# Optimization experiments

Measured on AMD Instinct MI355X. Metric: run time of the kernel, lower is better.

The kernel has to match this reference:

```python
import jax, jax.numpy as jnp
import numpy as np

N_USERS = 50000
N_ITEMS = 50000
N_NODES = N_USERS + N_ITEMS
EMBED_DIM = 64
N_INTER = 2_000_000
SSL_RATIO = 0.5
SSL_TEMP = 0.5
SSL_REG = 0.5
BATCH = 2048


def _make_subgraph(tu, ti, seed):
    """Edge-dropout (aug_type=1) + symmetric normalization, as COO arrays."""
    rng = np.random.default_rng(seed)
    keep = rng.choice(N_INTER, int(N_INTER * (1.0 - SSL_RATIO)), replace=False)
    u = tu[keep]
    i = ti[keep] + N_USERS
    rows = np.concatenate([u, i])          # symmetrize: A + A^T
    cols = np.concatenate([i, u])
    deg = np.bincount(rows, minlength=N_NODES).astype(np.float32)
    dinv = np.where(deg > 0, 1.0 / np.sqrt(deg), 0.0).astype(np.float32)
    vals = dinv[rows] * dinv[cols]         # D^-1/2 A D^-1/2
    return (jnp.asarray(rows, jnp.int32), jnp.asarray(cols, jnp.int32),
            jnp.asarray(vals, jnp.float32))


def setup_inputs() -> dict:
    key = jax.random.key(0)
    k1, k2, k3, k4 = jax.random.split(key, 4)
    rng = np.random.default_rng(0)
    tu = rng.integers(0, N_USERS, N_INTER)
    ti = rng.integers(0, N_ITEMS, N_INTER)
    rows1, cols1, vals1 = _make_subgraph(tu, ti, 1)
    rows2, cols2, vals2 = _make_subgraph(tu, ti, 2)
    return {
        "user_emb": jax.random.normal(k1, (N_USERS, EMBED_DIM), jnp.float32) * 0.1,
        "item_emb": jax.random.normal(k2, (N_ITEMS, EMBED_DIM), jnp.float32) * 0.1,
        "rows1": rows1, "cols1": cols1, "vals1": vals1,
        "rows2": rows2, "cols2": cols2, "vals2": vals2,
        "nodes_u": jax.random.randint(k3, (BATCH,), 0, N_USERS, jnp.int32),
        "nodes_i": jax.random.randint(k4, (BATCH,), 0, N_ITEMS, jnp.int32),
    }


def _spmm(rows, cols, vals, x):
    # sparse (n_nodes x n_nodes) @ dense (n_nodes x d) via gather + segment_sum
    return jax.ops.segment_sum(vals[:, None] * x[cols], rows, num_segments=N_NODES)


def _l2norm(x):
    return x / jnp.maximum(jnp.linalg.norm(x, axis=1, keepdims=True), 1e-12)


def _info_nce(emb1_all, emb2_all, idx, temp):
    z1 = _l2norm(emb1_all[idx])            # [B, d]
    z2 = _l2norm(emb2_all[idx])            # [B, d]
    zall = _l2norm(emb2_all)               # [N, d]
    pos = jnp.exp(jnp.sum(z1 * z2, axis=1) / temp)           # [B]
    ttl = jnp.sum(jnp.exp(jnp.dot(z1, zall.T) / temp), axis=1)  # [B]
    return -jnp.sum(jnp.log(pos / ttl))


def reference(user_emb, item_emb, rows1, cols1, vals1, rows2, cols2, vals2,
              nodes_u, nodes_i):
    ego = jnp.concatenate([user_emb, item_emb], axis=0)   # [N_NODES, d]
    # NOTE: in the original source the propagation matmul sits *after* the
    # layer loop (indentation bug), so exactly one SpMM layer is applied and
    # the stacked mean is (ego + A @ ego) / 2. We reproduce that faithfully.
    e1 = 0.5 * (ego + _spmm(rows1, cols1, vals1, ego))
    e2 = 0.5 * (ego + _spmm(rows2, cols2, vals2, ego))
    u1, i1 = e1[:N_USERS], e1[N_USERS:]
    u2, i2 = e2[:N_USERS], e2[N_USERS:]
    ssl_loss_user = _info_nce(u1, u2, nodes_u, SSL_TEMP)
    ssl_loss_item = _info_nce(i1, i2, nodes_i, SSL_TEMP)
    return SSL_REG * (ssl_loss_user + ssl_loss_item)
```

## Files before the change

### kernel.cpp

```cpp
#include <hip/hip_runtime.h>
#include <hip/hip_bf16.h>
#include <hip/hip_fp16.h>
#include <math.h>

#define N_USERS 50000
#define N_ITEMS 50000
#define N_NODES 100000
#define DIM 64
#define BATCH 2048
#define SLOTS 4096

#define BROWS 128
#define NBUK 782
#define CAPB 4096
#define SUBCAP 1024
#define BCHUNK 8192
#define BINTHREADS 1024

#define TTL_PRESCALE 2.8853900817779268f

using frag_ab = __attribute__((ext_vector_type(8))) short;
using frag_cd = __attribute__((ext_vector_type(4))) float;
typedef unsigned long long u64;
typedef unsigned int u32;


__device__ __forceinline__ float wave_reduce_sum(float v) {
#pragma unroll
  for (int off = 32; off > 0; off >>= 1)
    v += __shfl_xor(v, off, 64);
  return v;
}

__device__ __forceinline__ const float* ego_row(const float* ue, const float* ie, int n) {
  return (n < N_USERS) ? (ue + (size_t)n * DIM) : (ie + (size_t)(n - N_USERS) * DIM);
}

__device__ __forceinline__ ushort f2bf(float x) {
  __hip_bfloat16 h = __float2bfloat16(x);
  return *(ushort*)&h;
}

__device__ __forceinline__ float bf2f(ushort u) {
  return __uint_as_float(((unsigned)u) << 16);
}

__device__ __forceinline__ float exp2_native(float x) {
  float y;
  asm volatile("v_exp_f32 %0, %1" : "=v"(y) : "v"(x));
  return y;
}


__global__ void build_map_kernel(const int* __restrict__ nu, const int* __restrict__ ni,
                                 int* __restrict__ map) {
  int s = blockIdx.x * blockDim.x + threadIdx.x;
  if (s >= SLOTS) return;
  int n = (s < BATCH) ? nu[s] : (N_USERS + ni[s - BATCH]);
  map[n] = s;
}

__global__ __launch_bounds__(BINTHREADS) void bin_kernel(
    const int* __restrict__ rows, const int* __restrict__ cols,
    int* __restrict__ bcur, u32* __restrict__ rec, int nE) {
  __shared__ int lofs[NBUK];
  int tid = threadIdx.x;
  int sub = blockIdx.x & 3;
  int e0 = blockIdx.x * BCHUNK;
  int nHere = nE - e0;
  if (nHere > BCHUNK) nHere = BCHUNK;

  for (int i = tid; i < NBUK; i += BINTHREADS) lofs[i] = 0;
  __syncthreads();

  for (int i = tid; i < nHere; i += BINTHREADS)
    atomicAdd(&lofs[rows[e0 + i] >> 7], 1);
  __syncthreads();

  for (int b = tid; b < NBUK; b += BINTHREADS) {
    int c = lofs[b];
    lofs[b] = c ? atomicAdd(&bcur[(b * 4 + sub) * 16], c) : 0;
  }
  __syncthreads();

  for (int i = tid; i < nHere; i += BINTHREADS) {
    int r = rows[e0 + i];
    int b = r >> 7;
    int p = atomicAdd(&lofs[b], 1);
    if (p < SUBCAP)
      rec[((size_t)b << 12) + sub * SUBCAP + p] =
          ((u32)(r & 127) << 17) | (u32)cols[e0 + i];
  }
}

__global__ __launch_bounds__(256) void sort_kernel(
    const int* __restrict__ bcur, const u32* __restrict__ rec,
    u32* __restrict__ rec2, int* __restrict__ base, int* __restrict__ endv) {
  __shared__ int hist[BROWS];
  __shared__ int hcur[BROWS];
  int b = blockIdx.x;
  int tid = threadIdx.x;
  int cnt[4];
#pragma unroll
  for (int j = 0; j < 4; j++) {
    int c = bcur[(b * 4 + j) * 16];
    cnt[j] = (c < SUBCAP) ? c : SUBCAP;
  }
  size_t gb = (size_t)b << 12;

  if (tid < BROWS) hist[tid] = 0;
  __syncthreads();

  u32 myrec[CAPB / 256];
#pragma unroll
  for (int i = 0; i < CAPB / 256; i++) {
    int k = tid + i * 256;
    u32 u = ((k & (SUBCAP - 1)) < cnt[i >> 2]) ? rec[gb + k] : ~0u;
    myrec[i] = u;
    if (u != ~0u) atomicAdd(&hist[(u >> 17) & 127], 1);
  }
  __syncthreads();

  int wave = tid >> 6, lane = tid & 63;
  if (wave == 0) {
    int v0 = hist[lane], v1 = hist[lane + 64];
    int s0 = v0, s1 = v1;
#pragma unroll
    for (int off = 1; off < 64; off <<= 1) {
      int t0 = __shfl_up(s0, off, 64);
      if (lane >= off) s0 += t0;
      int t1 = __shfl_up(s1, off, 64);
      if (lane >= off) s1 += t1;
    }
    int tot0 = __shfl(s0, 63, 64);
    int e0 = s0 - v0;
    int e1 = tot0 + s1 - v1;
    hcur[lane] = e0;
    hcur[lane + 64] = e1;
    int gb32 = b * CAPB;
    int n0 = b * BROWS;
    if (n0 + lane < N_NODES) {
      base[n0 + lane] = gb32 + e0;
      endv[n0 + lane] = gb32 + e0 + v0;
    }
    if (n0 + lane + 64 < N_NODES) {
      base[n0 + lane + 64] = gb32 + e1;
      endv[n0 + lane + 64] = gb32 + e1 + v1;
    }
  }
  __syncthreads();

#pragma unroll
  for (int i = 0; i < CAPB / 256; i++) {
    u32 u = myrec[i];
    if (u != ~0u) {
      int rl = (u >> 17) & 127;
      int pos = atomicAdd(&hcur[rl], 1);
      rec2[gb + pos] = u & 0x1FFFF;
    }
  }
}

__global__ void ego2bf_kernel(const float* __restrict__ ue, const float* __restrict__ ie,
                              const int* __restrict__ base, const int* __restrict__ endv,
                              ushort* __restrict__ xb, ushort* __restrict__ xbp) {
  int t = blockIdx.x * blockDim.x + threadIdx.x;
  const int TOT = N_NODES * DIM / 4;
  if (t >= TOT) return;
  const int UH = N_USERS * DIM / 4;
  float4 f = (t < UH) ? ((const float4*)ue)[t] : ((const float4*)ie)[t - UH];
  ushort4 o;
  o.x = f2bf(f.x); o.y = f2bf(f.y); o.z = f2bf(f.z); o.w = f2bf(f.w);
  ((ushort4*)xb)[t] = o;
  int node = t >> 4;
  int d = endv[node] - base[node];
  float dc = (d > 0) ? rsqrtf((float)d) : 0.f;
  ushort4 p;
  p.x = f2bf(f.x * dc); p.y = f2bf(f.y * dc); p.z = f2bf(f.z * dc); p.w = f2bf(f.w * dc);
  ((ushort4*)xbp)[t] = p;
}

__global__ __launch_bounds__(256) void spmm_csr_norm_kernel(
    const int* __restrict__ base, const int* __restrict__ endv,
    const u32* __restrict__ rec2, const ushort* __restrict__ xbp,
    const float* __restrict__ ue, const float* __restrict__ ie,
    ushort* __restrict__ zallb) {
  int n = blockIdx.x * 4 + (threadIdx.x >> 6);
  if (n >= N_NODES) return;
  int lane = threadIdx.x & 63;
  int half = lane >> 5;
  int sl = lane & 31;
  int b = base[n];
  int d = endv[n] - b;
  const u32* rp = rec2 + b;
  float a0 = 0.f, a1 = 0.f;
  int k = half;
  for (; k + 6 < d; k += 8) {
    u32 c0 = rp[k], c1 = rp[k + 2], c2 = rp[k + 4], c3 = rp[k + 6];
    u32 u0 = *(const u32*)(xbp + ((size_t)c0 << 6) + 2 * sl);
    u32 u1 = *(const u32*)(xbp + ((size_t)c1 << 6) + 2 * sl);
    u32 u2 = *(const u32*)(xbp + ((size_t)c2 << 6) + 2 * sl);
    u32 u3 = *(const u32*)(xbp + ((size_t)c3 << 6) + 2 * sl);
    a0 += (__uint_as_float(u0 << 16) + __uint_as_float(u1 << 16)) +
          (__uint_as_float(u2 << 16) + __uint_as_float(u3 << 16));
    a1 += (__uint_as_float(u0 & 0xFFFF0000u) + __uint_as_float(u1 & 0xFFFF0000u)) +
          (__uint_as_float(u2 & 0xFFFF0000u) + __uint_as_float(u3 & 0xFFFF0000u));
  }
  for (; k < d; k += 2) {
    u32 c = rp[k];
    u32 u = *(const u32*)(xbp + ((size_t)c << 6) + 2 * sl);
    a0 += __uint_as_float(u << 16);
    a1 += __uint_as_float(u & 0xFFFF0000u);
  }
  a0 += __shfl_xor(a0, 32, 64);
  a1 += __shfl_xor(a1, 32, 64);

  float dinv = (d > 0) ? rsqrtf((float)d) : 0.f;
  a0 *= dinv;
  a1 *= dinv;

  const float* eg = ego_row(ue, ie, n);
  float2 e2 = *(const float2*)(eg + 2 * sl);
  float w0 = 0.5f * (e2.x + a0);
  float w1 = 0.5f * (e2.y + a1);
  float ss = w0 * w0 + w1 * w1;
#pragma unroll
  for (int off = 16; off > 0; off >>= 1)
    ss += __shfl_xor(ss, off, 64);
  float inv = 1.f / fmaxf(sqrtf(ss), 1e-12f);
  if (half == 0) {
    ushort2 oz;
    oz.x = f2bf(w0 * inv);
    oz.y = f2bf(w1 * inv);
    *(ushort2*)(zallb + (size_t)n * DIM + 2 * sl) = oz;
  }
}

__global__ __launch_bounds__(256) void graph1_fused_kernel(
    const int* __restrict__ rows, const int* __restrict__ cols,
    const float* __restrict__ vals, const int* __restrict__ map,
    const ushort* __restrict__ xb, float* __restrict__ z1acc, int nE) {
  __shared__ int lcount;
  __shared__ int hcol[256];
  __shared__ float hval[256];
  __shared__ int hslot[256];
  int tid = threadIdx.x;
  if (tid == 0) lcount = 0;
  __syncthreads();
  int e = blockIdx.x * 256 + tid;
  if (e < nE) {
    int r = rows[e];
    int s = map[r];
    if (s >= 0) {
      int pos = atomicAdd(&lcount, 1);
      hcol[pos] = cols[e];
      hval[pos] = vals[e];
      hslot[pos] = s;
    }
  }
  __syncthreads();
  int n = lcount;
  int wave = tid >> 6, lane = tid & 63;
  for (int k = wave; k < n; k += 4) {
    int c = hcol[k];
    float v = hval[k];
    int s = hslot[k];
    float x = bf2f(xb[(size_t)c * DIM + lane]);
    unsafeAtomicAdd(&z1acc[(size_t)s * DIM + lane], v * x);
  }
}

__global__ void gather1_kernel(const float* __restrict__ ue, const float* __restrict__ ie,
                               const int* __restrict__ nu, const int* __restrict__ ni,
                               const int* __restrict__ map, const float* __restrict__ z1acc,
                               const ushort* __restrict__ zallb, ushort* __restrict__ z1b,
                               float* __restrict__ posdot) {
  int s = blockIdx.x * 4 + (threadIdx.x >> 6);
  if (s >= SLOTS) return;
  int lane = threadIdx.x & 63;
  int n = (s < BATCH) ? nu[s] : (N_USERS + ni[s - BATCH]);
  int fs = map[n];
  const float* e = ego_row(ue, ie, n);
  float v = 0.5f * (e[lane] + z1acc[(size_t)fs * DIM + lane]);
  float ss = wave_reduce_sum(v * v);
  float z = v / fmaxf(sqrtf(ss), 1e-12f);
  z1b[(size_t)s * DIM + lane] = f2bf(z * TTL_PRESCALE);
  float dp = wave_reduce_sum(z * bf2f(zallb[(size_t)n * DIM + lane]));
  if (lane == 0) posdot[s] = dp;
}

#define TTL_STRIPS 125
#define TTL_CHUNKS 25
#define TTL_RB 16
__global__ __launch_bounds__(512) void ttl_mfma_kernel(const ushort* __restrict__ z1b,
                                                       const ushort* __restrict__ zallb,
                                                       float* __restrict__ partial) {
  __shared__ int4 sB[TTL_CHUNKS * 128];
  int bid = blockIdx.x;
  int strip = (bid & 7) + 8 * (bid >> 7);
  int rb = (bid >> 3) & 15;
  if (strip >= TTL_STRIPS) return;
  int tid = threadIdx.x;
  int wave = tid >> 6, lane = tid & 63;
  int r0 = rb * 256 + wave * 32;
  int side = (rb * 256) >> 11;
  const ushort* zs = zallb + (size_t)side * N_USERS * DIM;

  int m = lane & 15, q = lane >> 4;
  const ushort* ar0 = z1b + (size_t)(r0 + m) * DIM + q * 8;
  frag_ab a00 = *(const frag_ab*)ar0;
  frag_ab a01 = *(const frag_ab*)(ar0 + 32);
  const ushort* ar1 = ar0 + 16 * DIM;
  frag_ab a10 = *(const frag_ab*)ar1;
  frag_ab a11 = *(const frag_ab*)(ar1 + 32);

  int j0 = strip * (TTL_CHUNKS * 16);
  const char* bbase = (const char*)(zs + (size_t)j0 * DIM);

  for (int i = tid; i < TTL_CHUNKS * 128; i += 512) {
    int off = i * 16;
    int swz = off ^ (((off >> 7) & 7) << 4);
    *(int4*)((char*)sB + swz) = *(const int4*)(bbase + off);
  }
  __syncthreads();

  int swl = (m & 7) << 4;
  int o0 = (m * 128 + q * 16) ^ swl;
  int o1 = (m * 128 + 64 + q * 16) ^ swl;

  float racc[8] = {0.f, 0.f, 0.f, 0.f, 0.f, 0.f, 0.f, 0.f};

  for (int c = 0; c < TTL_CHUNKS; c++) {
    const char* sb = (const char*)sB + c * 2048;
    frag_ab b0 = *(const frag_ab*)(sb + o0);
    frag_ab b1 = *(const frag_ab*)(sb + o1);
    frag_cd acc0 = {}, acc1 = {};
    acc0 = __builtin_amdgcn_mfma_f32_16x16x32_bf16(a00, b0, acc0, 0, 0, 0);
    acc0 = __builtin_amdgcn_mfma_f32_16x16x32_bf16(a01, b1, acc0, 0, 0, 0);
    acc1 = __builtin_amdgcn_mfma_f32_16x16x32_bf16(a10, b0, acc1, 0, 0, 0);
    acc1 = __builtin_amdgcn_mfma_f32_16x16x32_bf16(a11, b1, acc1, 0, 0, 0);
#pragma unroll
    for (int r = 0; r < 4; r++) {
      racc[r] += exp2_native(acc0[r]);
      racc[4 + r] += exp2_native(acc1[r]);
    }
  }

  float* pw = partial + (size_t)strip * SLOTS;
#pragma unroll
  for (int h = 0; h < 2; h++) {
#pragma unroll
    for (int r = 0; r < 4; r++) {
      float v = racc[h * 4 + r];
      v += __shfl_xor(v, 1, 64);
      v += __shfl_xor(v, 2, 64);
      v += __shfl_xor(v, 4, 64);
      v += __shfl_xor(v, 8, 64);
      if (m == 0) pw[r0 + h * 16 + q * 4 + r] = v;
    }
  }
}

__global__ void final_kernel(const float* __restrict__ partial,
                             const float* __restrict__ posdot,
                             float* __restrict__ out) {
  int row = blockIdx.x * blockDim.x + threadIdx.x;
  float t = 0.f;
  for (int s = 0; s < TTL_STRIPS; s++)
    t += partial[(size_t)s * SLOTS + row];
  float v = 0.5f * logf(t) - posdot[row];
  v = wave_reduce_sum(v);
  if ((threadIdx.x & 63) == 0) atomicAdd(out, v);
}


extern "C" void kernel_launch(void* const* d_in, const int* in_sizes, int n_in,
                              void* d_out, int out_size, void* d_ws, size_t ws_size,
                              hipStream_t stream) {
  const float* ue = (const float*)d_in[0];
  const float* ie = (const float*)d_in[1];
  const int* rows1 = (const int*)d_in[2];
  const int* cols1 = (const int*)d_in[3];
  const float* vals1 = (const float*)d_in[4];
  const int* rows2 = (const int*)d_in[5];
  const int* cols2 = (const int*)d_in[6];
  const int* nu = (const int*)d_in[8];
  const int* ni = (const int*)d_in[9];
  int nE1 = in_sizes[2], nE2 = in_sizes[5];

  char* ws = (char*)d_ws;
  size_t o = 0;
  auto carve = [&](size_t bytes) {
    char* p = ws + o;
    o += (bytes + 255) & ~(size_t)255;
    return p;
  };
  int* map = (int*)carve(N_NODES * 4);
  float* z1acc = (float*)carve((size_t)SLOTS * DIM * 4);
  float* partial = (float*)carve((size_t)TTL_STRIPS * SLOTS * 4);
  float* posdot = (float*)carve(SLOTS * 4);
  ushort* zallb = (ushort*)carve((size_t)N_NODES * DIM * 2);
  ushort* z1b = (ushort*)carve((size_t)SLOTS * DIM * 2);
  ushort* xb = (ushort*)carve((size_t)N_NODES * DIM * 2);
  ushort* xbp = (ushort*)carve((size_t)N_NODES * DIM * 2);
  int* bcur = (int*)carve((size_t)NBUK * 4 * 16 * 4);
  int* base = (int*)carve(N_NODES * 4);
  int* endv = (int*)carve(N_NODES * 4);
  u32* rec = (u32*)carve((size_t)NBUK * CAPB * 4);
  u32* rec2 = (u32*)carve((size_t)NBUK * CAPB * 4);
  float* out = (float*)d_out;

  hipMemsetAsync(map, 0xFF, N_NODES * 4, stream);
  hipMemsetAsync(bcur, 0, (size_t)NBUK * 4 * 16 * 4, stream);
  hipMemsetAsync(z1acc, 0, (size_t)SLOTS * DIM * 4, stream);
  hipMemsetAsync(out, 0, sizeof(float), stream);

  build_map_kernel<<<16, 256, 0, stream>>>(nu, ni, map);
  bin_kernel<<<(nE2 + BCHUNK - 1) / BCHUNK, BINTHREADS, 0, stream>>>(rows2, cols2, bcur, rec, nE2);
  sort_kernel<<<NBUK, 256, 0, stream>>>(bcur, rec, rec2, base, endv);
  ego2bf_kernel<<<(N_NODES * DIM / 4 + 255) / 256, 256, 0, stream>>>(ue, ie, base, endv, xb, xbp);
  spmm_csr_norm_kernel<<<(N_NODES + 3) / 4, 256, 0, stream>>>(base, endv, rec2, xbp, ue, ie, zallb);
  graph1_fused_kernel<<<(nE1 + 255) / 256, 256, 0, stream>>>(rows1, cols1, vals1, map, xb, z1acc, nE1);
  gather1_kernel<<<SLOTS / 4, 256, 0, stream>>>(ue, ie, nu, ni, map, z1acc, zallb, z1b, posdot);
  ttl_mfma_kernel<<<2048, 512, 0, stream>>>(z1b, zallb, partial);
  final_kernel<<<SLOTS / 256, 256, 0, stream>>>(partial, posdot, out);
}
```

Measured before the change: 315.2 us.

## Merge bf16 conversion into binning, scaling into sort, and graph1 into SpMM launch

The separate ego-to-bf16 kernel is removed. The plain bf16 conversion now runs as extra blocks of the binning launch, and the degree-scaled copy is produced at the tail of the sort kernel from the per-row histogram it already holds. The graph-1 gather/atomic kernel is merged into the graph-2 CSR SpMM launch as additional blocks, so the two independent workloads can overlap. This cuts two launches and the endv/base reads in the conversion step. In exchange, xbp is now rounded to bf16 twice, and the fused launches mix block types with different shared-memory needs.

```diff
diff --git a/kernel.cpp b/kernel.cpp
--- a/kernel.cpp
+++ b/kernel.cpp
@@ -16,8 +16,11 @@
 #define SUBCAP 1024
 #define BCHUNK 8192
 #define BINTHREADS 1024
+#define XB_BLOCKS 1563
 
 #define TTL_PRESCALE 2.8853900817779268f
+
+#define SPMM_BLOCKS (N_NODES / 4)
 
 using frag_ab = __attribute__((ext_vector_type(8))) short;
 using frag_cd = __attribute__((ext_vector_type(4))) float;
@@ -60,9 +63,24 @@
   map[n] = s;
 }
 
-__global__ __launch_bounds__(BINTHREADS) void bin_kernel(
+__global__ __launch_bounds__(BINTHREADS) void bin_xb_kernel(
     const int* __restrict__ rows, const int* __restrict__ cols,
-    int* __restrict__ bcur, u32* __restrict__ rec, int nE) {
+    const float* __restrict__ ue, const float* __restrict__ ie,
+    int* __restrict__ bcur, u32* __restrict__ rec, ushort* __restrict__ xb,
+    int nE, int nBin) {
+  if ((int)blockIdx.x >= nBin) {
+    int t = (blockIdx.x - nBin) * BINTHREADS + threadIdx.x;
+    const int TOT = N_NODES * DIM / 4;
+    if (t < TOT) {
+      const int UH = N_USERS * DIM / 4;
+      float4 f = (t < UH) ? ((const float4*)ue)[t] : ((const float4*)ie)[t - UH];
+      ushort4 o;
+      o.x = f2bf(f.x); o.y = f2bf(f.y); o.z = f2bf(f.z); o.w = f2bf(f.w);
+      ((ushort4*)xb)[t] = o;
+    }
+    return;
+  }
+
   __shared__ int lofs[NBUK];
   int tid = threadIdx.x;
   int sub = blockIdx.x & 3;
@@ -95,7 +113,8 @@
 
 __global__ __launch_bounds__(256) void sort_kernel(
     const int* __restrict__ bcur, const u32* __restrict__ rec,
-    u32* __restrict__ rec2, int* __restrict__ base, int* __restrict__ endv) {
+    u32* __restrict__ rec2, int* __restrict__ base, int* __restrict__ endv,
+    const ushort* __restrict__ xb, ushort* __restrict__ xbp) {
   __shared__ int hist[BROWS];
   __shared__ int hcur[BROWS];
   int b = blockIdx.x;
@@ -159,35 +178,72 @@
       rec2[gb + pos] = u & 0x1FFFF;
     }
   }
-}
-
-__global__ void ego2bf_kernel(const float* __restrict__ ue, const float* __restrict__ ie,
-                              const int* __restrict__ base, const int* __restrict__ endv,
-                              ushort* __restrict__ xb, ushort* __restrict__ xbp) {
-  int t = blockIdx.x * blockDim.x + threadIdx.x;
-  const int TOT = N_NODES * DIM / 4;
-  if (t >= TOT) return;
-  const int UH = N_USERS * DIM / 4;
-  float4 f = (t < UH) ? ((const float4*)ue)[t] : ((const float4*)ie)[t - UH];
-  ushort4 o;
-  o.x = f2bf(f.x); o.y = f2bf(f.y); o.z = f2bf(f.z); o.w = f2bf(f.w);
-  ((ushort4*)xb)[t] = o;
-  int node = t >> 4;
-  int d = endv[node] - base[node];
-  float dc = (d > 0) ? rsqrtf((float)d) : 0.f;
-  ushort4 p;
-  p.x = f2bf(f.x * dc); p.y = f2bf(f.y * dc); p.z = f2bf(f.z * dc); p.w = f2bf(f.w * dc);
-  ((ushort4*)xbp)[t] = p;
-}
-
-__global__ __launch_bounds__(256) void spmm_csr_norm_kernel(
+
+  int r = tid >> 1;
+  int n = b * BROWS + r;
+  if (n < N_NODES) {
+    int dg = hist[r];
+    float dc = (dg > 0) ? rsqrtf((float)dg) : 0.f;
+    const ushort4* src = (const ushort4*)(xb + (size_t)n * DIM + (tid & 1) * 32);
+    ushort4* dst = (ushort4*)(xbp + (size_t)n * DIM + (tid & 1) * 32);
+#pragma unroll
+    for (int j = 0; j < 8; j++) {
+      ushort4 v = src[j];
+      ushort4 p;
+      p.x = f2bf(bf2f(v.x) * dc);
+      p.y = f2bf(bf2f(v.y) * dc);
+      p.z = f2bf(bf2f(v.z) * dc);
+      p.w = f2bf(bf2f(v.w) * dc);
+      dst[j] = p;
+    }
+  }
+}
+
+__global__ __launch_bounds__(256) void spmm_graph1_kernel(
     const int* __restrict__ base, const int* __restrict__ endv,
     const u32* __restrict__ rec2, const ushort* __restrict__ xbp,
     const float* __restrict__ ue, const float* __restrict__ ie,
-    ushort* __restrict__ zallb) {
-  int n = blockIdx.x * 4 + (threadIdx.x >> 6);
+    ushort* __restrict__ zallb,
+    const int* __restrict__ rows1, const int* __restrict__ cols1,
+    const float* __restrict__ vals1, const int* __restrict__ map,
+    const ushort* __restrict__ xb, float* __restrict__ z1acc, int nE1) {
+  __shared__ int lcount;
+  __shared__ int hcol[256];
+  __shared__ float hval[256];
+  __shared__ int hslot[256];
+  int bid = blockIdx.x;
+  int tid = threadIdx.x;
+
+  if (bid >= SPMM_BLOCKS) {
+    if (tid == 0) lcount = 0;
+    __syncthreads();
+    int e = (bid - SPMM_BLOCKS) * 256 + tid;
+    if (e < nE1) {
+      int r = rows1[e];
+      int s = map[r];
+      if (s >= 0) {
+        int pos = atomicAdd(&lcount, 1);
+        hcol[pos] = cols1[e];
+        hval[pos] = vals1[e];
+        hslot[pos] = s;
+      }
+    }
+    __syncthreads();
+    int cnt = lcount;
+    int wave = tid >> 6, lane = tid & 63;
+    for (int k = wave; k < cnt; k += 4) {
+      int c = hcol[k];
+      float v = hval[k];
+      int s = hslot[k];
+      float x = bf2f(xb[(size_t)c * DIM + lane]);
+      unsafeAtomicAdd(&z1acc[(size_t)s * DIM + lane], v * x);
+    }
+    return;
+  }
+
+  int n = bid * 4 + (tid >> 6);
   if (n >= N_NODES) return;
-  int lane = threadIdx.x & 63;
+  int lane = tid & 63;
   int half = lane >> 5;
   int sl = lane & 31;
   int b = base[n];
@@ -233,40 +289,6 @@
     oz.x = f2bf(w0 * inv);
     oz.y = f2bf(w1 * inv);
     *(ushort2*)(zallb + (size_t)n * DIM + 2 * sl) = oz;
-  }
-}
-
-__global__ __launch_bounds__(256) void graph1_fused_kernel(
-    const int* __restrict__ rows, const int* __restrict__ cols,
-    const float* __restrict__ vals, const int* __restrict__ map,
-    const ushort* __restrict__ xb, float* __restrict__ z1acc, int nE) {
-  __shared__ int lcount;
-  __shared__ int hcol[256];
-  __shared__ float hval[256];
-  __shared__ int hslot[256];
-  int tid = threadIdx.x;
-  if (tid == 0) lcount = 0;
-  __syncthreads();
-  int e = blockIdx.x * 256 + tid;
-  if (e < nE) {
-    int r = rows[e];
-    int s = map[r];
-    if (s >= 0) {
-      int pos = atomicAdd(&lcount, 1);
-      hcol[pos] = cols[e];
-      hval[pos] = vals[e];
-      hslot[pos] = s;
-    }
-  }
-  __syncthreads();
-  int n = lcount;
-  int wave = tid >> 6, lane = tid & 63;
-  for (int k = wave; k < n; k += 4) {
-    int c = hcol[k];
-    float v = hval[k];
-    int s = hslot[k];
-    float x = bf2f(xb[(size_t)c * DIM + lane]);
-    unsafeAtomicAdd(&z1acc[(size_t)s * DIM + lane], v * x);
   }
 }
 
@@ -416,11 +438,13 @@
   hipMemsetAsync(out, 0, sizeof(float), stream);
 
   build_map_kernel<<<16, 256, 0, stream>>>(nu, ni, map);
-  bin_kernel<<<(nE2 + BCHUNK - 1) / BCHUNK, BINTHREADS, 0, stream>>>(rows2, cols2, bcur, rec, nE2);
-  sort_kernel<<<NBUK, 256, 0, stream>>>(bcur, rec, rec2, base, endv);
-  ego2bf_kernel<<<(N_NODES * DIM / 4 + 255) / 256, 256, 0, stream>>>(ue, ie, base, endv, xb, xbp);
-  spmm_csr_norm_kernel<<<(N_NODES + 3) / 4, 256, 0, stream>>>(base, endv, rec2, xbp, ue, ie, zallb);
-  graph1_fused_kernel<<<(nE1 + 255) / 256, 256, 0, stream>>>(rows1, cols1, vals1, map, xb, z1acc, nE1);
+  int nBin = (nE2 + BCHUNK - 1) / BCHUNK;
+  bin_xb_kernel<<<nBin + XB_BLOCKS, BINTHREADS, 0, stream>>>(
+      rows2, cols2, ue, ie, bcur, rec, xb, nE2, nBin);
+  sort_kernel<<<NBUK, 256, 0, stream>>>(bcur, rec, rec2, base, endv, xb, xbp);
+  int g1Blocks = (nE1 + 255) / 256;
+  spmm_graph1_kernel<<<SPMM_BLOCKS + g1Blocks, 256, 0, stream>>>(
+      base, endv, rec2, xbp, ue, ie, zallb, rows1, cols1, vals1, map, xb, z1acc, nE1);
   gather1_kernel<<<SLOTS / 4, 256, 0, stream>>>(ue, ie, nu, ni, map, z1acc, zallb, z1b, posdot);
   ttl_mfma_kernel<<<2048, 512, 0, stream>>>(z1b, zallb, partial);
   final_kernel<<<SLOTS / 256, 256, 0, stream>>>(partial, posdot, out);
```

Result: faster. 302.8 us (-3.9%).
